# Optimization experiments

Hardware: AMD Instinct MI355X
Metric: run time of the kernel (lower is better)

Reference implementation:

```python
import jax, jax.numpy as jnp
import numpy as np

# Dims (see shape_source)
B, C_IN, H, W = 32, 256, 56, 56
O, J = 256, 64            # out_channels, in_connects (sparse in-channel subset per out channel)
KH, KW = 3, 3
STRIDE = (1, 1)
PAD = (1, 1)


def setup_inputs() -> dict:
    key = jax.random.key(0)
    k1, k2 = jax.random.split(key)
    x = jax.random.normal(k1, (B, C_IN, H, W), dtype=jnp.float32)
    # init_rand_indices: each out channel samples in_connects distinct in-channels
    rng = np.random.default_rng(0)
    w_idx = jnp.asarray(
        np.stack([rng.permutation(C_IN)[:J] for _ in range(O)]), dtype=jnp.int32
    )  # [O, J]
    # reset_parameters: uniform(-stdv, +stdv), stdv = 1/sqrt(in_connects * kh * kw)
    stdv = 1.0 / np.sqrt(J * KH * KW)
    w_vals = jax.random.uniform(k2, (O, J, KH, KW), dtype=jnp.float32,
                                minval=-stdv, maxval=stdv)
    return {"x": x, "w_vals": w_vals, "w_idx": w_idx}


def reference(x, w_vals, w_idx):
    # Sparse conv: out[b,o] = sum_j conv(x[:, w_idx[o,j]], w_vals[o,j]).
    # Equivalent math: scatter sparse weights into a dense [O, C_in, KH, KW]
    # kernel (zeros on unselected channels) and run one dense conv.
    dense_w = jnp.zeros((O, C_IN, KH, KW), dtype=w_vals.dtype)
    dense_w = dense_w.at[jnp.arange(O)[:, None], w_idx].set(w_vals)
    out = jax.lax.conv_general_dilated(
        x, dense_w,
        window_strides=STRIDE,
        padding=[(PAD[0], PAD[0]), (PAD[1], PAD[1])],
        dimension_numbers=("NCHW", "OIHW", "NCHW"),
    )  # [B, O, H, W]
    return out
```

## Files before the change

### kernel.cpp

```cpp
#include <hip/hip_runtime.h>
#include <hip/hip_bf16.h>


typedef __attribute__((ext_vector_type(8))) short bf16x8;
typedef __attribute__((ext_vector_type(4))) float f32x4;

#define WD_BYTES 1179648
#define XP_BYTES 55115776
#define WS_NEED  (WD_BYTES + XP_BYTES)
#define ABUF 32768
#define BBUF 28672
#define BOFF 65536
#define LDS_TOT 122880

__global__ __launch_bounds__(256) void preproc(
    const float* __restrict__ x, const float* __restrict__ wv,
    const int* __restrict__ widx, __hip_bfloat16* __restrict__ wd,
    __hip_bfloat16* __restrict__ xp)
{
    int bid = blockIdx.x;
    int tid = threadIdx.x;
    if (bid >= 1792) {
        int o = bid - 1792;
        int j = tid & 63;
        if (tid < 64) {
#pragma unroll
            for (int k = 0; k < 9; ++k)
                reinterpret_cast<float2*>(wd + (size_t)k * 65536 + o * 256)[j] =
                    float2{0.f, 0.f};
        }
        __syncthreads();
        if (tid < 64) {
            int cin = widx[o * 64 + j];
            const float* src = wv + (size_t)(o * 64 + j) * 9;
#pragma unroll
            for (int k = 0; k < 9; ++k)
                wd[(size_t)k * 65536 + o * 256 + cin] = __float2bfloat16(src[k]);
        }
        return;
    }
    int b = bid / 56, h = bid - (bid / 56) * 56;
    __shared__ __hip_bfloat16 tile[56][264];
    int c = tid;
    const float* src = x + ((size_t)(b * 256 + c)) * 3136 + h * 56;
    float vals[56];
#pragma unroll
    for (int i = 0; i < 14; ++i) {
        float4 v = *reinterpret_cast<const float4*>(src + i * 4);
        vals[i*4+0] = v.x; vals[i*4+1] = v.y; vals[i*4+2] = v.z; vals[i*4+3] = v.w;
    }
#pragma unroll
    for (int w = 0; w < 56; ++w) tile[w][c] = __float2bfloat16(vals[w]);

    char* rowb = (char*)xp + (((size_t)b * 58 + (h + 1)) * 58) * 512;
    if (tid < 64)        reinterpret_cast<double*>(rowb)[tid] = 0.0;
    else if (tid < 128)  *reinterpret_cast<double*>(rowb + 57 * 512 + (tid - 64) * 8) = 0.0;
    if (h == 0) {
        char* r0 = (char*)xp + (((size_t)b * 58 + 0) * 58) * 512;
        for (int i = tid; i < 58 * 64; i += 256) reinterpret_cast<double*>(r0)[i] = 0.0;
    }
    if (h == 55) {
        char* r57 = (char*)xp + (((size_t)b * 58 + 57) * 58) * 512;
        for (int i = tid; i < 58 * 64; i += 256) reinterpret_cast<double*>(r57)[i] = 0.0;
    }

    __syncthreads();
    char* obase = (char*)xp + (((size_t)b * 58 + (h + 1)) * 58) * 512;
#pragma unroll
    for (int k = 0; k < 7; ++k) {
        int i = tid + k * 256;
        int w = i >> 5, cc = i & 31;
        bf16x8 v = *reinterpret_cast<const bf16x8*>(&tile[w][cc * 8]);
        *reinterpret_cast<bf16x8*>(obase + (size_t)(w + 1) * 512 + cc * 16) = v;
    }
}


__device__ __forceinline__ void gload_lds16(const void* g, void* l) {
    __builtin_amdgcn_global_load_lds(
        (const __attribute__((address_space(1))) void*)g,
        (__attribute__((address_space(3))) void*)l, 16, 0, 0);
}

template<int BB, int J>
__device__ __forceinline__ void stage_a(const char* wdB, char* smem, int wid,
                                        int sa_off, int aoff) {
    gload_lds16(wdB + aoff + J * 64 * 512 + sa_off,
                smem + BB * ABUF + (J * 64 + wid * 8) * 128);
}

template<int BB, int J>
__device__ __forceinline__ void stage_b(const char* xpB, char* smem, int wid,
                                        int pbJ, int boff) {
    gload_lds16(xpB + pbJ + boff,
                smem + BOFF + BB * BBUF + (J * 64 + wid * 8) * 128);
}

__device__ __forceinline__ int pixoff(int p) {
    int b = p / 3136; int r = p - b * 3136;
    int h = r / 56;   int w = r - h * 56;
    return ((b * 58 + h + 1) * 58 + (w + 1)) * 512;
}

__device__ __forceinline__ int aoff_t(int t) {
    return (t >> 2) * 131072 + (t & 3) * 128;
}
__device__ __forceinline__ int boff_t(int t) {
    int k9 = t >> 2; int kh = k9 / 3; int kw = k9 - 3 * kh;
    return ((kh - 1) * 58 + (kw - 1)) * 512 + (t & 3) * 128;
}

#define BAR() __builtin_amdgcn_s_barrier()
#define VMCNT0() asm volatile("s_waitcnt vmcnt(0)" ::: "memory")

template<int U>
__device__ __forceinline__ void ktile(
    const char* wdB, const char* xpB, char* smem,
    int wid, int wr, int wc, int a_rb, int xq0, int xq1, int sa_off,
    int pb0, int pb1, int pb2, int pb3,
    int tn, f32x4 (&acc)[4][7])
{
    const int aBase = U * ABUF + wr * 64 * 128 + a_rb;
    const int bBase = BOFF + U * BBUF + wc * 112 * 128 + a_rb;

    bf16x8 af0[4], bf0[7], af1[4], bf1[7];
    af0[0] = *(const bf16x8*)(smem + aBase + xq0);
#pragma unroll
    for (int ni = 0; ni < 7; ++ni)
        bf0[ni] = *(const bf16x8*)(smem + bBase + ni * 16 * 128 + xq0);
#pragma unroll
    for (int mi = 1; mi < 4; ++mi)
        af0[mi] = *(const bf16x8*)(smem + aBase + mi * 16 * 128 + xq0);

    const int an = aoff_t(tn), bn = boff_t(tn);
    stage_a<1-U,0>(wdB, smem, wid, sa_off, an);
    stage_a<1-U,1>(wdB, smem, wid, sa_off, an);
    stage_a<1-U,2>(wdB, smem, wid, sa_off, an);
    stage_a<1-U,3>(wdB, smem, wid, sa_off, an);
    stage_b<1-U,0>(xpB, smem, wid, pb0, bn);
    stage_b<1-U,1>(xpB, smem, wid, pb1, bn);
    stage_b<1-U,2>(xpB, smem, wid, pb2, bn);
    if (wid < 4) stage_b<1-U,3>(xpB, smem, wid, pb3, bn);

    af1[0] = *(const bf16x8*)(smem + aBase + xq1);
#pragma unroll
    for (int ni = 0; ni < 7; ++ni)
        bf1[ni] = *(const bf16x8*)(smem + bBase + ni * 16 * 128 + xq1);
#pragma unroll
    for (int mi = 1; mi < 4; ++mi)
        af1[mi] = *(const bf16x8*)(smem + aBase + mi * 16 * 128 + xq1);

    __builtin_amdgcn_s_setprio(1);
#pragma unroll
    for (int mi = 0; mi < 4; ++mi)
#pragma unroll
        for (int ni = 0; ni < 7; ++ni)
            acc[mi][ni] = __builtin_amdgcn_mfma_f32_16x16x32_bf16(
                af0[mi], bf0[ni], acc[mi][ni], 0, 0, 0);
#pragma unroll
    for (int mi = 0; mi < 4; ++mi)
#pragma unroll
        for (int ni = 0; ni < 7; ++ni)
            acc[mi][ni] = __builtin_amdgcn_mfma_f32_16x16x32_bf16(
                af1[mi], bf1[ni], acc[mi][ni], 0, 0, 0);
    __builtin_amdgcn_s_setprio(0);

    VMCNT0();
    BAR();
}

__global__ __launch_bounds__(512, 2) void sparse_conv_mfma224(
    const __hip_bfloat16* __restrict__ wd, const __hip_bfloat16* __restrict__ xp,
    float* __restrict__ out)
{
    extern __shared__ char smem[];
    const char* wdB = (const char*)wd;
    const char* xpB = (const char*)xp;

    const int bid = blockIdx.x;
    const int nt = (bid & 7) * 56 + (bid >> 3);

    const int t = threadIdx.x;
    const int lane = t & 63, wid = t >> 6;
    const int wr = wid >> 1, wc = wid & 1;

    const int axor = (((lane & 7) ^ (lane >> 3)) * 16);
    const int sa_off = (wid * 8 + (lane >> 3)) * 512 + axor;
    const int prow = wid * 8 + (lane >> 3);
    const int pb0 = pixoff(nt * 224 +   0 + prow) + axor;
    const int pb1 = pixoff(nt * 224 +  64 + prow) + axor;
    const int pb2 = pixoff(nt * 224 + 128 + prow) + axor;
    const int pb3 = (wid < 4) ? (pixoff(nt * 224 + 192 + prow) + axor) : 0;

    const int a_rb = (lane & 15) * 128;
    const int xq0 = (((lane >> 4)) ^ (lane & 7)) * 16;
    const int xq1 = ((4 + (lane >> 4)) ^ (lane & 7)) * 16;

    f32x4 acc[4][7] = {};

    {
        const int a0 = aoff_t(0), b0 = boff_t(0);
        stage_a<0,0>(wdB, smem, wid, sa_off, a0);
        stage_a<0,1>(wdB, smem, wid, sa_off, a0);
        stage_a<0,2>(wdB, smem, wid, sa_off, a0);
        stage_a<0,3>(wdB, smem, wid, sa_off, a0);
        stage_b<0,0>(xpB, smem, wid, pb0, b0);
        stage_b<0,1>(xpB, smem, wid, pb1, b0);
        stage_b<0,2>(xpB, smem, wid, pb2, b0);
        if (wid < 4) stage_b<0,3>(xpB, smem, wid, pb3, b0);
        VMCNT0();
        BAR();
    }

    for (int it = 0; it < 18; ++it) {
        const int t1 = 2 * it + 1;
        int t2 = t1 + 1; if (t2 == 36) t2 = 0;
        ktile<0>(wdB, xpB, smem, wid, wr, wc, a_rb, xq0, xq1, sa_off,
                 pb0, pb1, pb2, pb3, t1, acc);
        ktile<1>(wdB, xpB, smem, wid, wr, wc, a_rb, xq0, xq1, sa_off,
                 pb0, pb1, pb2, pb3, t2, acc);
    }

#pragma unroll
    for (int n = 0; n < 7; ++n) {
        int p0 = nt * 224 + wc * 112 + n * 16;
        int pb = p0 / 3136;
        int rem0 = p0 - pb * 3136;
#pragma unroll
        for (int m = 0; m < 4; ++m) {
            int o = wr * 64 + m * 16 + (lane >> 4) * 4;
            float* dst = out + ((size_t)(pb * 256 + o)) * 3136 + rem0 + (lane & 15);
#pragma unroll
            for (int r = 0; r < 4; ++r) dst[(size_t)r * 3136] = acc[m][n][r];
        }
    }
}


__global__ __launch_bounds__(256) void sparse_conv_direct(
    const float* __restrict__ x, const float* __restrict__ wv,
    const int* __restrict__ widx, float* __restrict__ out)
{
    const int bid = blockIdx.x;
    const int b = bid >> 8, o = bid & 255;
    const int tid = threadIdx.x;
    __shared__ float plane[58 * 60];
    const int rt = tid >> 3, ct = tid & 7;
    const int r0 = rt * 2, c0 = ct * 7;
    const bool active = (rt < 28);
    float acc[2][7];
#pragma unroll
    for (int i = 0; i < 2; ++i)
#pragma unroll
        for (int c = 0; c < 7; ++c) acc[i][c] = 0.f;
    const float* xb = x + (size_t)b * 256 * 3136;
    const int* idxp = widx + o * 64;
    const float* wp0 = wv + (size_t)o * 64 * 9;
    for (int j = 0; j < 64; ++j) {
        const int cin = idxp[j];
        const float* src = xb + cin * 3136;
        __syncthreads();
        for (int i = tid; i < 58 * 58; i += 256) {
            const int r = i / 58, c = i - r * 58;
            const int h = r - 1, w = c - 1;
            float v = 0.f;
            if ((unsigned)h < 56u && (unsigned)w < 56u) v = src[h * 56 + w];
            plane[r * 60 + c] = v;
        }
        float wreg[9];
#pragma unroll
        for (int k = 0; k < 9; ++k) wreg[k] = wp0[j * 9 + k];
        __syncthreads();
        if (active) {
            float rows[4][9];
#pragma unroll
            for (int dr = 0; dr < 4; ++dr)
#pragma unroll
                for (int cc = 0; cc < 9; ++cc)
                    rows[dr][cc] = plane[(r0 + dr) * 60 + (c0 + cc)];
#pragma unroll
            for (int i = 0; i < 2; ++i)
#pragma unroll
                for (int cc = 0; cc < 7; ++cc) {
                    float s = acc[i][cc];
#pragma unroll
                    for (int kh = 0; kh < 3; ++kh)
#pragma unroll
                        for (int kw = 0; kw < 3; ++kw)
                            s += rows[i + kh][cc + kw] * wreg[kh * 3 + kw];
                    acc[i][cc] = s;
                }
        }
    }
    if (active) {
        float* op = out + (size_t)bid * 3136;
#pragma unroll
        for (int i = 0; i < 2; ++i)
#pragma unroll
            for (int cc = 0; cc < 7; ++cc)
                op[(r0 + i) * 56 + (c0 + cc)] = acc[i][cc];
    }
}

extern "C" void kernel_launch(void* const* d_in, const int* in_sizes, int n_in,
                              void* d_out, int out_size, void* d_ws, size_t ws_size,
                              hipStream_t stream) {
    const float* x    = (const float*)d_in[0];
    const float* wv   = (const float*)d_in[1];
    const int*   widx = (const int*)d_in[2];
    float* out = (float*)d_out;
    (void)in_sizes; (void)n_in; (void)out_size;

    if (ws_size < (size_t)WS_NEED) {
        sparse_conv_direct<<<dim3(32 * 256), dim3(256), 0, stream>>>(x, wv, widx, out);
        return;
    }

    __hip_bfloat16* wd = (__hip_bfloat16*)d_ws;
    __hip_bfloat16* xp = (__hip_bfloat16*)((char*)d_ws + WD_BYTES);

    preproc<<<dim3(32 * 56 + 256), dim3(256), 0, stream>>>(x, wv, widx, wd, xp);

    (void)hipFuncSetAttribute((const void*)sparse_conv_mfma224,
                              hipFuncAttributeMaxDynamicSharedMemorySize, LDS_TOT);
    sparse_conv_mfma224<<<dim3(448), dim3(512), LDS_TOT, stream>>>(wd, xp, out);
}
```

Before: 148.4 us.

## Stage input halo once per channel slice and reuse it across all 3x3 taps

Instead of re-fetching a shifted B tile from global memory for each of the 9 kernel taps, the kernel now loads a 6-row padded halo of the input for a 64-channel slice into LDS once. It then reads the tap-shifted pixels from LDS using a row shift and an XOR swizzle. This cuts global/L2 traffic for the activation operand by about 9x per slice. The cost is that only A is double-buffered, and each slice change adds a serialized halo reload with a barrier, so that load is exposed rather than overlapped. LDS footprint drops slightly.

```diff
diff --git a/kernel.cpp b/kernel.cpp
--- a/kernel.cpp
+++ b/kernel.cpp
@@ -8,10 +8,9 @@
 #define WD_BYTES 1179648
 #define XP_BYTES 55115776
 #define WS_NEED  (WD_BYTES + XP_BYTES)
-#define ABUF 32768
-#define BBUF 28672
-#define BOFF 65536
-#define LDS_TOT 122880
+#define ABUF  32768
+#define BHOFF 65536
+#define LDS_TOT (65536 + 49152)
 
 __global__ __launch_bounds__(256) void preproc(
     const float* __restrict__ x, const float* __restrict__ wv,
@@ -82,92 +81,23 @@
         (__attribute__((address_space(3))) void*)l, 16, 0, 0);
 }
 
-template<int BB, int J>
-__device__ __forceinline__ void stage_a(const char* wdB, char* smem, int wid,
-                                        int sa_off, int aoff) {
-    gload_lds16(wdB + aoff + J * 64 * 512 + sa_off,
-                smem + BB * ABUF + (J * 64 + wid * 8) * 128);
-}
-
-template<int BB, int J>
-__device__ __forceinline__ void stage_b(const char* xpB, char* smem, int wid,
-                                        int pbJ, int boff) {
-    gload_lds16(xpB + pbJ + boff,
-                smem + BOFF + BB * BBUF + (J * 64 + wid * 8) * 128);
-}
-
-__device__ __forceinline__ int pixoff(int p) {
-    int b = p / 3136; int r = p - b * 3136;
-    int h = r / 56;   int w = r - h * 56;
-    return ((b * 58 + h + 1) * 58 + (w + 1)) * 512;
-}
-
-__device__ __forceinline__ int aoff_t(int t) {
-    return (t >> 2) * 131072 + (t & 3) * 128;
-}
-__device__ __forceinline__ int boff_t(int t) {
-    int k9 = t >> 2; int kh = k9 / 3; int kw = k9 - 3 * kh;
-    return ((kh - 1) * 58 + (kw - 1)) * 512 + (t & 3) * 128;
+__device__ __forceinline__ void stage_a4(const char* wdB, char* smem, int dstA,
+                                         int wid, int sa_off, int aoff) {
+#pragma unroll
+    for (int J = 0; J < 4; ++J)
+        gload_lds16(wdB + aoff + J * 32768 + sa_off,
+                    smem + dstA + (J * 64 + wid * 8) * 128);
+}
+
+__device__ __forceinline__ void stage_bh6(const char* xpOcs, char* smem, int wid,
+                                          const int (&srcp)[6]) {
+#pragma unroll
+    for (int j = 0; j < 6; ++j)
+        gload_lds16(xpOcs + srcp[j], smem + BHOFF + j * 8192 + wid * 1024);
 }
 
 #define BAR() __builtin_amdgcn_s_barrier()
 #define VMCNT0() asm volatile("s_waitcnt vmcnt(0)" ::: "memory")
-
-template<int U>
-__device__ __forceinline__ void ktile(
-    const char* wdB, const char* xpB, char* smem,
-    int wid, int wr, int wc, int a_rb, int xq0, int xq1, int sa_off,
-    int pb0, int pb1, int pb2, int pb3,
-    int tn, f32x4 (&acc)[4][7])
-{
-    const int aBase = U * ABUF + wr * 64 * 128 + a_rb;
-    const int bBase = BOFF + U * BBUF + wc * 112 * 128 + a_rb;
-
-    bf16x8 af0[4], bf0[7], af1[4], bf1[7];
-    af0[0] = *(const bf16x8*)(smem + aBase + xq0);
-#pragma unroll
-    for (int ni = 0; ni < 7; ++ni)
-        bf0[ni] = *(const bf16x8*)(smem + bBase + ni * 16 * 128 + xq0);
-#pragma unroll
-    for (int mi = 1; mi < 4; ++mi)
-        af0[mi] = *(const bf16x8*)(smem + aBase + mi * 16 * 128 + xq0);
-
-    const int an = aoff_t(tn), bn = boff_t(tn);
-    stage_a<1-U,0>(wdB, smem, wid, sa_off, an);
-    stage_a<1-U,1>(wdB, smem, wid, sa_off, an);
-    stage_a<1-U,2>(wdB, smem, wid, sa_off, an);
-    stage_a<1-U,3>(wdB, smem, wid, sa_off, an);
-    stage_b<1-U,0>(xpB, smem, wid, pb0, bn);
-    stage_b<1-U,1>(xpB, smem, wid, pb1, bn);
-    stage_b<1-U,2>(xpB, smem, wid, pb2, bn);
-    if (wid < 4) stage_b<1-U,3>(xpB, smem, wid, pb3, bn);
-
-    af1[0] = *(const bf16x8*)(smem + aBase + xq1);
-#pragma unroll
-    for (int ni = 0; ni < 7; ++ni)
-        bf1[ni] = *(const bf16x8*)(smem + bBase + ni * 16 * 128 + xq1);
-#pragma unroll
-    for (int mi = 1; mi < 4; ++mi)
-        af1[mi] = *(const bf16x8*)(smem + aBase + mi * 16 * 128 + xq1);
-
-    __builtin_amdgcn_s_setprio(1);
-#pragma unroll
-    for (int mi = 0; mi < 4; ++mi)
-#pragma unroll
-        for (int ni = 0; ni < 7; ++ni)
-            acc[mi][ni] = __builtin_amdgcn_mfma_f32_16x16x32_bf16(
-                af0[mi], bf0[ni], acc[mi][ni], 0, 0, 0);
-#pragma unroll
-    for (int mi = 0; mi < 4; ++mi)
-#pragma unroll
-        for (int ni = 0; ni < 7; ++ni)
-            acc[mi][ni] = __builtin_amdgcn_mfma_f32_16x16x32_bf16(
-                af1[mi], bf1[ni], acc[mi][ni], 0, 0, 0);
-    __builtin_amdgcn_s_setprio(0);
-
-    VMCNT0();
-    BAR();
-}
 
 __global__ __launch_bounds__(512, 2) void sparse_conv_mfma224(
     const __hip_bfloat16* __restrict__ wd, const __hip_bfloat16* __restrict__ xp,
@@ -186,46 +116,100 @@
 
     const int axor = (((lane & 7) ^ (lane >> 3)) * 16);
     const int sa_off = (wid * 8 + (lane >> 3)) * 512 + axor;
-    const int prow = wid * 8 + (lane >> 3);
-    const int pb0 = pixoff(nt * 224 +   0 + prow) + axor;
-    const int pb1 = pixoff(nt * 224 +  64 + prow) + axor;
-    const int pb2 = pixoff(nt * 224 + 128 + prow) + axor;
-    const int pb3 = (wid < 4) ? (pixoff(nt * 224 + 192 + prow) + axor) : 0;
 
     const int a_rb = (lane & 15) * 128;
     const int xq0 = (((lane >> 4)) ^ (lane & 7)) * 16;
     const int xq1 = ((4 + (lane >> 4)) ^ (lane & 7)) * 16;
+    const int wrOff = wr * 8192;
+
+    const int p0 = nt * 224;
+    const int bImg = p0 / 3136;
+    const int r0 = (p0 - bImg * 3136) / 56;
+    const char* xpO = xpB + (size_t)((bImg * 58 + r0) * 58) * 512;
+
+    int srcp[6];
+#pragma unroll
+    for (int j = 0; j < 6; ++j) {
+        int beta = j * 8192 + wid * 1024 + lane * 16;
+        int rb = beta >> 7;
+        int c  = (beta >> 4) & 7;
+        srcp[j] = (rb < 348) ? (rb * 512 + ((c ^ (rb & 7)) << 4)) : 0;
+    }
+
+    int rowpl[7];
+#pragma unroll
+    for (int n = 0; n < 7; ++n) {
+        int q = wc * 112 + n * 16 + (lane & 15);
+        int qr = q / 56;
+        rowpl[n] = qr * 58 + (q - qr * 56);
+    }
+    const int g4 = lane >> 4;
 
     f32x4 acc[4][7] = {};
 
-    {
-        const int a0 = aoff_t(0), b0 = boff_t(0);
-        stage_a<0,0>(wdB, smem, wid, sa_off, a0);
-        stage_a<0,1>(wdB, smem, wid, sa_off, a0);
-        stage_a<0,2>(wdB, smem, wid, sa_off, a0);
-        stage_a<0,3>(wdB, smem, wid, sa_off, a0);
-        stage_b<0,0>(xpB, smem, wid, pb0, b0);
-        stage_b<0,1>(xpB, smem, wid, pb1, b0);
-        stage_b<0,2>(xpB, smem, wid, pb2, b0);
-        if (wid < 4) stage_b<0,3>(xpB, smem, wid, pb3, b0);
+    stage_bh6(xpO, smem, wid, srcp);
+    stage_a4(wdB, smem, 0, wid, sa_off, 0);
+    VMCNT0();
+    BAR();
+
+    int k9 = 0, cs = 0, shift = 0;
+    for (int g = 0; g < 36; ++g) {
+        int k9n = k9 + 1, csn = cs;
+        if (k9n == 9) { k9n = 0; csn = cs + 1; if (csn == 4) csn = 0; }
+        stage_a4(wdB, smem, ((g + 1) & 1) * ABUF, wid, sa_off,
+                 k9n * 131072 + csn * 128);
+
+        const int abase = (g & 1) * ABUF + wrOff + a_rb;
+        bf16x8 af0[4], af1[4], bf0[7], bf1[7];
+#pragma unroll
+        for (int mi = 0; mi < 4; ++mi) {
+            af0[mi] = *(const bf16x8*)(smem + abase + mi * 2048 + xq0);
+            af1[mi] = *(const bf16x8*)(smem + abase + mi * 2048 + xq1);
+        }
+#pragma unroll
+        for (int n = 0; n < 7; ++n) {
+            int roff = rowpl[n] + shift;
+            int ba = BHOFF + (roff << 7) + ((g4 ^ (roff & 7)) << 4);
+            bf0[n] = *(const bf16x8*)(smem + ba);
+            bf1[n] = *(const bf16x8*)(smem + (ba ^ 64));
+        }
+
+        __builtin_amdgcn_s_setprio(1);
+#pragma unroll
+        for (int mi = 0; mi < 4; ++mi)
+#pragma unroll
+            for (int ni = 0; ni < 7; ++ni)
+                acc[mi][ni] = __builtin_amdgcn_mfma_f32_16x16x32_bf16(
+                    af0[mi], bf0[ni], acc[mi][ni], 0, 0, 0);
+#pragma unroll
+        for (int mi = 0; mi < 4; ++mi)
+#pragma unroll
+            for (int ni = 0; ni < 7; ++ni)
+                acc[mi][ni] = __builtin_amdgcn_mfma_f32_16x16x32_bf16(
+                    af1[mi], bf1[ni], acc[mi][ni], 0, 0, 0);
+        __builtin_amdgcn_s_setprio(0);
+
         VMCNT0();
         BAR();
-    }
-
-    for (int it = 0; it < 18; ++it) {
-        const int t1 = 2 * it + 1;
-        int t2 = t1 + 1; if (t2 == 36) t2 = 0;
-        ktile<0>(wdB, xpB, smem, wid, wr, wc, a_rb, xq0, xq1, sa_off,
-                 pb0, pb1, pb2, pb3, t1, acc);
-        ktile<1>(wdB, xpB, smem, wid, wr, wc, a_rb, xq0, xq1, sa_off,
-                 pb0, pb1, pb2, pb3, t2, acc);
+
+        if (k9n == 0) {
+            if (csn != 0) {
+                stage_bh6(xpO + csn * 128, smem, wid, srcp);
+                VMCNT0();
+                BAR();
+            }
+            shift = 0;
+        } else {
+            shift += ((k9n % 3) == 0) ? 56 : 1;
+        }
+        k9 = k9n; cs = csn;
     }
 
 #pragma unroll
     for (int n = 0; n < 7; ++n) {
-        int p0 = nt * 224 + wc * 112 + n * 16;
-        int pb = p0 / 3136;
-        int rem0 = p0 - pb * 3136;
+        int p = nt * 224 + wc * 112 + n * 16;
+        int pb = p / 3136;
+        int rem0 = p - pb * 3136;
 #pragma unroll
         for (int m = 0; m < 4; ++m) {
             int o = wr * 64 + m * 16 + (lane >> 4) * 4;
```

Result: no change. 150.0 us (+1.1%).
